# Performance work log

Hardware: AMD Instinct MI355X
Metric: run time of the kernel (lower is better)

Reference implementation:

```python
import jax, jax.numpy as jnp
import numpy as np

D_QUERY = 512
D_AUDIO = 512
D_OUT = 512
B, HW, S = 16, 4096, 1024


def setup_inputs() -> dict:
    key = jax.random.key(0)
    ks = jax.random.split(key, 8)
    sc_q = 1.0 / np.sqrt(D_QUERY)
    sc_a = 1.0 / np.sqrt(D_AUDIO)
    return {
        "x": jax.random.normal(ks[0], (B, HW, D_QUERY), dtype=jnp.float32),
        "audio_embed": jax.random.normal(ks[1], (B, S, D_AUDIO), dtype=jnp.float32),
        "Wq": jax.random.uniform(ks[2], (D_QUERY, D_OUT), jnp.float32, -sc_q, sc_q),
        "bq": jax.random.uniform(ks[3], (D_OUT,), jnp.float32, -sc_q, sc_q),
        "Wk": jax.random.uniform(ks[4], (D_AUDIO, D_OUT), jnp.float32, -sc_a, sc_a),
        "bk": jax.random.uniform(ks[5], (D_OUT,), jnp.float32, -sc_a, sc_a),
        "Wv": jax.random.uniform(ks[6], (D_AUDIO, D_OUT), jnp.float32, -sc_a, sc_a),
        "bv": jax.random.uniform(ks[7], (D_OUT,), jnp.float32, -sc_a, sc_a),
    }


def reference(x, audio_embed, Wq, bq, Wk, bk, Wv, bv):
    # Linear projections (nn.Linear: y = x @ W^T + b; we store W already transposed)
    Q = x @ Wq + bq                      # [B, HW, D_OUT]
    K = audio_embed @ Wk + bk            # [B, S, D_OUT]
    V = audio_embed @ Wv + bv            # [B, S, D_OUT]
    scale = 1.0 / (K.shape[-1] ** 0.5)   # divide by sqrt(d_out), per source
    scores = jnp.einsum("bnd,bsd->bns", Q, K) * scale  # [B, HW, S]
    attn = jax.nn.softmax(scores, axis=-1)
    return jnp.einsum("bns,bsd->bnd", attn, V)         # [B, HW, D_OUT]
```

## Files before the change

kernel.cpp:

```cpp
#include <hip/hip_runtime.h>
#include <hip/hip_bf16.h>

typedef __attribute__((ext_vector_type(8))) short bf16x8;
typedef __attribute__((ext_vector_type(4))) float f32x4;
typedef __attribute__((ext_vector_type(4))) unsigned short ushort4v;

#define AS1 __attribute__((address_space(1)))
#define AS3 __attribute__((address_space(3)))

__device__ __forceinline__ float bf_bits_to_f(short s) {
  unsigned int u = ((unsigned int)(unsigned short)s) << 16;
  union { unsigned int u; float f; } c; c.u = u; return c.f;
}
__device__ __forceinline__ unsigned short f_to_bf_bits(float f) {
  union { float f; unsigned int u; } c; c.f = f;
  unsigned int r = c.u + 0x7FFFu + ((c.u >> 16) & 1u);
  return (unsigned short)(r >> 16);
}

__device__ __forceinline__ int fsw(int row) { return ((row >> 1) & 3) << 4; }

__global__ __launch_bounds__(256) void cvt_bf16_kernel(const float* __restrict__ in,
                                                       unsigned short* __restrict__ out,
                                                       long n) {
  const long nchunks = n >> 2;
  const long stride = (long)gridDim.x * 256;
  for (long c = (long)blockIdx.x * 256 + threadIdx.x; c < nchunks; c += stride) {
    f32x4 v = *(const f32x4*)(in + c * 4);
    ushort4v o;
    o[0] = f_to_bf_bits(v[0]); o[1] = f_to_bf_bits(v[1]);
    o[2] = f_to_bf_bits(v[2]); o[3] = f_to_bf_bits(v[3]);
    *(ushort4v*)(out + c * 4) = o;
  }
}

__global__ __launch_bounds__(256) void transpose1_kernel(
    const float* __restrict__ W, unsigned short* __restrict__ T) {
  __shared__ float t[32][33];
  const int tx = threadIdx.x & 31, ty = threadIdx.x >> 5;
  const int n0 = blockIdx.x * 32, k0 = blockIdx.y * 32;
#pragma unroll
  for (int j = 0; j < 4; ++j)
    t[ty + 8 * j][tx] = W[(long)(k0 + ty + 8 * j) * 512 + n0 + tx];
  __syncthreads();
#pragma unroll
  for (int j = 0; j < 4; ++j)
    T[(long)(n0 + ty + 8 * j) * 512 + k0 + tx] = f_to_bf_bits(t[tx][ty + 8 * j]);
}

__global__ __launch_bounds__(256) void wvec_kernel(const float* __restrict__ Wk,
                                                   const float* __restrict__ bq,
                                                   float* __restrict__ w, const float s) {
  const int q = blockIdx.x * 4 + (threadIdx.x >> 6);
  const int lane = threadIdx.x & 63;
  const float* row = Wk + (long)q * 512 + lane * 8;
  const f32x4 a0 = *(const f32x4*)row;
  const f32x4 a1 = *(const f32x4*)(row + 4);
  const f32x4 b0 = *(const f32x4*)(bq + lane * 8);
  const f32x4 b1 = *(const f32x4*)(bq + lane * 8 + 4);
  float d = a0[0]*b0[0] + a0[1]*b0[1] + a0[2]*b0[2] + a0[3]*b0[3]
          + a1[0]*b1[0] + a1[1]*b1[1] + a1[2]*b1[2] + a1[3]*b1[3];
  for (int off = 1; off < 64; off <<= 1) d += __shfl_xor(d, off);
  if (lane == 0) w[q] = d * s;
}

__global__ __launch_bounds__(256) void cvec_kernel(const float* __restrict__ audio,
                                                   const float* __restrict__ w,
                                                   float* __restrict__ cv) {
  const long row = (long)blockIdx.x * 4 + (threadIdx.x >> 6);
  const int lane = threadIdx.x & 63;
  const f32x4 a0 = *(const f32x4*)(audio + row * 512 + lane * 8);
  const f32x4 a1 = *(const f32x4*)(audio + row * 512 + lane * 8 + 4);
  const f32x4 w0 = *(const f32x4*)(w + lane * 8);
  const f32x4 w1 = *(const f32x4*)(w + lane * 8 + 4);
  float d = a0[0]*w0[0] + a0[1]*w0[1] + a0[2]*w0[2] + a0[3]*w0[3]
          + a1[0]*w1[0] + a1[1]*w1[1] + a1[2]*w1[2] + a1[3]*w1[3];
  for (int off = 1; off < 64; off <<= 1) d += __shfl_xor(d, off);
  if (lane == 0) cv[row] = d;
}

template <bool BIAS, bool TRANSOUT, bool AFP32>
__global__ __launch_bounds__(256) void gemm_kernel(
    const void* __restrict__ Aptr,
    const unsigned short* __restrict__ BT,
    const float* __restrict__ bias,
    unsigned short* __restrict__ Cout,
    const int K, const float scale,
    const long strideA, const long strideBT, const long strideC, const int ldc,
    const int nx, const int ny) {
  __shared__ unsigned short lds[8192];
  const int nwg = gridDim.x;
  const int chunk = nwg >> 3;
  const int bid = blockIdx.x;
  const int swz = (bid & 7) * chunk + (bid >> 3);
  const int bx = swz % nx;
  const int t1 = swz / nx;
  const int by = t1 % ny;
  const int bz = t1 / ny;

  const int tid = threadIdx.x;
  const int lane = tid & 63;
  const int wv = tid >> 6;
  const int wr = wv >> 1, wc = wv & 1;
  const unsigned short* Ab = (const unsigned short*)Aptr + (long)bz * strideA + (long)by * 128 * K;
  const float* Af = (const float*)Aptr + (long)bz * strideA + (long)by * 128 * K;
  const unsigned short* Bb = BT + (long)bz * strideBT + (long)bx * 128 * K;

  f32x4 acc[4][4];
#pragma unroll
  for (int m = 0; m < 4; ++m)
#pragma unroll
    for (int n = 0; n < 4; ++n) acc[m][n] = (f32x4){0.f, 0.f, 0.f, 0.f};

  const int r15 = lane & 15, g = lane >> 4;
  const int kiters = K >> 5;
  const int asw = fsw(r15);

  int arow[2], acs[2];
#pragma unroll
  for (int i = 0; i < 2; ++i) {
    const int c = i * 4 + wv;
    const int boff = c * 1024 + lane * 16;
    arow[i] = boff >> 6;
    acs[i] = (boff & 63) ^ fsw(arow[i]);
  }
  f32x4 pa[2][2];
  if (AFP32) {
#pragma unroll
    for (int i = 0; i < 2; ++i) {
      const float* s = Af + (long)arow[i] * K + (acs[i] >> 1);
      pa[i][0] = *(const f32x4*)s;
      pa[i][1] = *(const f32x4*)(s + 4);
    }
  }

  for (int kt = 0; kt < kiters; ++kt) {
#pragma unroll
    for (int i = 0; i < 2; ++i) {
      const int c = i * 4 + wv;
      const char* srcB = (const char*)Bb + (long)arow[i] * (K * 2) + kt * 64 + acs[i];
      __builtin_amdgcn_global_load_lds(
          (const AS1 void*)srcB, (AS3 void*)(lds + 4096 + c * 512), 16, 0, 0);
      if (!AFP32) {
        const char* srcA = (const char*)Ab + (long)arow[i] * (K * 2) + kt * 64 + acs[i];
        __builtin_amdgcn_global_load_lds(
            (const AS1 void*)srcA, (AS3 void*)(lds + c * 512), 16, 0, 0);
      }
    }
    if (AFP32) {
#pragma unroll
      for (int i = 0; i < 2; ++i) {
        const int c = i * 4 + wv;
        bf16x8 w;
#pragma unroll
        for (int e = 0; e < 4; ++e) {
          w[e] = (short)f_to_bf_bits(pa[i][0][e]);
          w[4 + e] = (short)f_to_bf_bits(pa[i][1][e]);
        }
        *(bf16x8*)&lds[c * 512 + lane * 8] = w;
      }
      if (kt < kiters - 1) {
#pragma unroll
        for (int i = 0; i < 2; ++i) {
          const float* s = Af + (long)arow[i] * K + (kt + 1) * 32 + (acs[i] >> 1);
          pa[i][0] = *(const f32x4*)s;
          pa[i][1] = *(const f32x4*)(s + 4);
        }
      }
    }
    __syncthreads();

    bf16x8 af[4], bf[4];
#pragma unroll
    for (int m = 0; m < 4; ++m)
      af[m] = *(const bf16x8*)((const char*)lds + (wr * 64 + m * 16 + r15) * 64 + (g * 16 ^ asw));
#pragma unroll
    for (int n = 0; n < 4; ++n)
      bf[n] = *(const bf16x8*)((const char*)lds + 8192 +
                               (wc * 64 + n * 16 + r15) * 64 + (g * 16 ^ asw));
#pragma unroll
    for (int m = 0; m < 4; ++m)
#pragma unroll
      for (int n = 0; n < 4; ++n)
        acc[m][n] = __builtin_amdgcn_mfma_f32_16x16x32_bf16(af[m], bf[n], acc[m][n], 0, 0, 0);
    __syncthreads();
  }

  const long crow0 = (long)by * 128 + wr * 64;
  const long ccol0 = (long)bx * 128 + wc * 64;
#pragma unroll
  for (int n = 0; n < 4; ++n) {
    const long col = ccol0 + n * 16 + r15;
    const float bv = BIAS ? bias[col] : 0.f;
#pragma unroll
    for (int m = 0; m < 4; ++m) {
      const f32x4 v = acc[m][n];
#pragma unroll
      for (int j = 0; j < 4; ++j) {
        const long row = crow0 + m * 16 + g * 4 + j;
        const float val = (v[j] + bv) * scale;
        const long idx = TRANSOUT ? (col * (long)ldc + row) : (row * (long)ldc + col);
        (Cout + (long)bz * strideC)[idx] = f_to_bf_bits(val);
      }
    }
  }
}

__global__ __launch_bounds__(256) void projdual_kernel(
    const float* __restrict__ audio,
    const unsigned short* __restrict__ wvt,
    const unsigned short* __restrict__ G,
    const float* __restrict__ bv,
    unsigned short* __restrict__ Vt,
    unsigned short* __restrict__ KMb) {
  __shared__ unsigned short lds[8192];
  const int nwg = gridDim.x;
  const int chunk = nwg >> 3;
  const int bid = blockIdx.x;
  const int swz = (bid & 7) * chunk + (bid >> 3);
  const int bx = swz & 7;
  const int t1 = swz >> 3;
  const int by = t1 & 7;
  const int bz = t1 >> 3;

  const int tid = threadIdx.x;
  const int lane = tid & 63;
  const int wv = tid >> 6;
  const int wr = wv >> 1, wc = wv & 1;
  const float* Af = audio + (long)bz * 1024 * 512 + (long)by * 128 * 512;
  const unsigned short* Bb = (bx < 4) ? (wvt + (long)bx * 128 * 512)
                                      : (G + (long)(bx - 4) * 128 * 512);

  f32x4 acc[4][4];
#pragma unroll
  for (int m = 0; m < 4; ++m)
#pragma unroll
    for (int n = 0; n < 4; ++n) acc[m][n] = (f32x4){0.f, 0.f, 0.f, 0.f};

  const int r15 = lane & 15, g = lane >> 4;
  const int asw = fsw(r15);

  int arow[2], acs[2];
#pragma unroll
  for (int i = 0; i < 2; ++i) {
    const int c = i * 4 + wv;
    const int boff = c * 1024 + lane * 16;
    arow[i] = boff >> 6;
    acs[i] = (boff & 63) ^ fsw(arow[i]);
  }
  f32x4 pa[2][2];
#pragma unroll
  for (int i = 0; i < 2; ++i) {
    const float* s = Af + (long)arow[i] * 512 + (acs[i] >> 1);
    pa[i][0] = *(const f32x4*)s;
    pa[i][1] = *(const f32x4*)(s + 4);
  }

  for (int kt = 0; kt < 16; ++kt) {
#pragma unroll
    for (int i = 0; i < 2; ++i) {
      const int c = i * 4 + wv;
      const char* srcB = (const char*)Bb + (long)arow[i] * 1024 + kt * 64 + acs[i];
      __builtin_amdgcn_global_load_lds(
          (const AS1 void*)srcB, (AS3 void*)(lds + 4096 + c * 512), 16, 0, 0);
    }
#pragma unroll
    for (int i = 0; i < 2; ++i) {
      const int c = i * 4 + wv;
      bf16x8 w;
#pragma unroll
      for (int e = 0; e < 4; ++e) {
        w[e] = (short)f_to_bf_bits(pa[i][0][e]);
        w[4 + e] = (short)f_to_bf_bits(pa[i][1][e]);
      }
      *(bf16x8*)&lds[c * 512 + lane * 8] = w;
    }
    if (kt < 15) {
#pragma unroll
      for (int i = 0; i < 2; ++i) {
        const float* s = Af + (long)arow[i] * 512 + (kt + 1) * 32 + (acs[i] >> 1);
        pa[i][0] = *(const f32x4*)s;
        pa[i][1] = *(const f32x4*)(s + 4);
      }
    }
    __syncthreads();

    bf16x8 af[4], bf[4];
#pragma unroll
    for (int m = 0; m < 4; ++m)
      af[m] = *(const bf16x8*)((const char*)lds + (wr * 64 + m * 16 + r15) * 64 + (g * 16 ^ asw));
#pragma unroll
    for (int n = 0; n < 4; ++n)
      bf[n] = *(const bf16x8*)((const char*)lds + 8192 +
                               (wc * 64 + n * 16 + r15) * 64 + (g * 16 ^ asw));
#pragma unroll
    for (int m = 0; m < 4; ++m)
#pragma unroll
      for (int n = 0; n < 4; ++n)
        acc[m][n] = __builtin_amdgcn_mfma_f32_16x16x32_bf16(af[m], bf[n], acc[m][n], 0, 0, 0);
    __syncthreads();
  }

  const long crow0 = (long)by * 128 + wr * 64;
  const long ccol0 = (long)bx * 128 + wc * 64;
#pragma unroll
  for (int n = 0; n < 4; ++n) {
    const long col = ccol0 + n * 16 + r15;
    const float bvv = (bx < 4) ? bv[col] : 0.f;
#pragma unroll
    for (int m = 0; m < 4; ++m) {
      const f32x4 v = acc[m][n];
#pragma unroll
      for (int j = 0; j < 4; ++j) {
        const long row = crow0 + m * 16 + g * 4 + j;
        const float val = v[j] + bvv;
        if (bx < 4)
          Vt[(long)bz * 512 * 1024 + col * 1024 + row] = f_to_bf_bits(val);
        else
          KMb[(long)bz * 1024 * 512 + row * 512 + (col - 512)] = f_to_bf_bits(val);
      }
    }
  }
}

template <bool EXPSTATS, bool DIVSTATS>
__global__ __launch_bounds__(512, 2) void gemm256_kernel(
    const unsigned short* __restrict__ A,
    const unsigned short* __restrict__ BT,
    void* __restrict__ Cout,
    const int K,
    const long strideA, const long strideBT, const long strideC, const int ldc,
    const int nx, const int ny, float* __restrict__ stats,
    const float* __restrict__ cbias) {
  __shared__ __align__(16) char halfb[4][32768];
  __shared__ float ssum[256][4];
  __shared__ float invl[256];

  const int nwg = gridDim.x;
  const int chunk = nwg >> 3;
  const int bid = blockIdx.x;
  const int swz = (bid & 7) * chunk + (bid >> 3);
  const int bx = swz % nx;
  const int t1 = swz / nx;
  const int by = t1 % ny;
  const int bz = t1 / ny;

  const int tid = threadIdx.x;
  const int lane = tid & 63;
  const int w = tid >> 6;
  const int wm = w >> 2, wn = w & 3;
  const int r15 = lane & 15, g = lane >> 4;
  const int asw = fsw(r15);

  const char* Abyt = (const char*)(A + (long)bz * strideA + (long)by * 256 * K);
  const char* Bbyt = (const char*)(BT + (long)bz * strideBT + (long)bx * 256 * K);
  const long rsb = (long)K * 2;

  if (DIVSTATS) {
    if (tid < 256) {
      const f32x4 s = *(const f32x4*)&stats[((long)bz * 4096 + (long)by * 256 + tid) * 4];
      invl[tid] = 1.f / (s[0] + s[1] + s[2] + s[3]);
    }
  }
  __builtin_amdgcn_sched_barrier(0);

  const int srow0 = tid >> 2;
  const int scol = ((tid & 3) << 4) ^ fsw(srow0);
  const long aoff0 = (long)srow0 * rsb + scol;
  const long aoff1 = (long)(srow0 + 128) * rsb + scol;
  const int dbase = tid * 16;

  auto stage = [&](int s) {
    char* h = halfb[s & 3];
    const long kb = (long)s * 64;
    __builtin_amdgcn_global_load_lds((const AS1 void*)(Abyt + aoff0 + kb),
                                     (AS3 void*)(h + dbase), 16, 0, 0);
    __builtin_amdgcn_global_load_lds((const AS1 void*)(Abyt + aoff1 + kb),
                                     (AS3 void*)(h + 8192 + dbase), 16, 0, 0);
    __builtin_amdgcn_global_load_lds((const AS1 void*)(Bbyt + aoff0 + kb),
                                     (AS3 void*)(h + 16384 + dbase), 16, 0, 0);
    __builtin_amdgcn_global_load_lds((const AS1 void*)(Bbyt + aoff1 + kb),
                                     (AS3 void*)(h + 24576 + dbase), 16, 0, 0);
  };

  f32x4 acc[8][4];
#pragma unroll
  for (int m = 0; m < 8; ++m)
#pragma unroll
    for (int n = 0; n < 4; ++n) acc[m][n] = (f32x4){0.f, 0.f, 0.f, 0.f};

  const int kslices = K >> 5;

  stage(0);
  stage(1);
  stage(2);
  asm volatile("s_waitcnt vmcnt(8)" ::: "memory");
  __builtin_amdgcn_s_barrier();
  __builtin_amdgcn_sched_barrier(0);

  for (int s = 0; s < kslices; ++s) {
    const char* hA = halfb[s & 3];
    const char* hB = halfb[s & 3] + 16384;
    bf16x8 fa[8], fb[4];
#pragma unroll
    for (int m = 0; m < 8; ++m)
      fa[m] = *(const bf16x8*)(hA + (wm * 128 + m * 16 + r15) * 64 + ((g * 16) ^ asw));
#pragma unroll
    for (int n = 0; n < 4; ++n)
      fb[n] = *(const bf16x8*)(hB + (wn * 64 + n * 16 + r15) * 64 + ((g * 16) ^ asw));
    __builtin_amdgcn_sched_barrier(0);
    if (s < kslices - 2) asm volatile("s_waitcnt vmcnt(4)" ::: "memory");
    else                 asm volatile("s_waitcnt vmcnt(0)" ::: "memory");
    __builtin_amdgcn_s_barrier();
    asm volatile("s_waitcnt lgkmcnt(0)" ::: "memory");
    __builtin_amdgcn_sched_barrier(0);
    if (s + 3 < kslices) stage(s + 3);
    __builtin_amdgcn_s_setprio(1);
#pragma unroll
    for (int m = 0; m < 8; ++m)
#pragma unroll
      for (int n = 0; n < 4; ++n)
        acc[m][n] = __builtin_amdgcn_mfma_f32_16x16x32_bf16(fa[m], fb[n], acc[m][n], 0, 0, 0);
    __builtin_amdgcn_s_setprio(0);
    __builtin_amdgcn_sched_barrier(0);
  }

  if (EXPSTATS) {
    float cb[4];
#pragma unroll
    for (int n = 0; n < 4; ++n)
      cb[n] = cbias[(long)bz * 1024 + (long)bx * 256 + wn * 64 + n * 16 + r15];
#pragma unroll
    for (int m = 0; m < 8; ++m)
#pragma unroll
      for (int n = 0; n < 4; ++n)
#pragma unroll
        for (int j = 0; j < 4; ++j) acc[m][n][j] = __expf(acc[m][n][j] + cb[n]);
#pragma unroll
    for (int m = 0; m < 8; ++m)
#pragma unroll
      for (int j = 0; j < 4; ++j) {
        float s = acc[m][0][j] + acc[m][1][j] + acc[m][2][j] + acc[m][3][j];
        s += __shfl_xor(s, 1);
        s += __shfl_xor(s, 2);
        s += __shfl_xor(s, 4);
        s += __shfl_xor(s, 8);
        if (r15 == 0) ssum[wm * 128 + m * 16 + g * 4 + j][wn] = s;
      }
    __syncthreads();
    if (tid < 256) {
      const float t = ssum[tid][0] + ssum[tid][1] + ssum[tid][2] + ssum[tid][3];
      stats[((long)bz * 4096 + (long)by * 256 + tid) * 4 + bx] = t;
    }
  }

  const long crow0 = (long)by * 256 + wm * 128;
  const long ccol0 = (long)bx * 256 + wn * 64;
#pragma unroll
  for (int m = 0; m < 8; ++m)
#pragma unroll
    for (int j = 0; j < 4; ++j) {
      const int rl = wm * 128 + m * 16 + g * 4 + j;
      const long row = crow0 + m * 16 + g * 4 + j;
#pragma unroll
      for (int n = 0; n < 4; ++n) {
        const long col = ccol0 + n * 16 + r15;
        if (EXPSTATS) {
          ((unsigned short*)Cout + (long)bz * strideC)[row * (long)ldc + col] =
              f_to_bf_bits(acc[m][n][j]);
        } else {
          const float sc = DIVSTATS ? invl[rl] : 1.f;
          ((float*)Cout + (long)bz * strideC)[row * (long)ldc + col] = acc[m][n][j] * sc;
        }
      }
    }
}

extern "C" void kernel_launch(void* const* d_in, const int* in_sizes, int n_in,
                              void* d_out, int out_size, void* d_ws, size_t ws_size,
                              hipStream_t stream) {
  (void)in_sizes; (void)n_in; (void)out_size; (void)ws_size;
  const float* x     = (const float*)d_in[0];
  const float* audio = (const float*)d_in[1];
  const float* Wq    = (const float*)d_in[2];
  const float* bq    = (const float*)d_in[3];
  const float* Wk    = (const float*)d_in[4];
  const float* bk    = (const float*)d_in[5];  (void)bk;
  const float* Wv    = (const float*)d_in[6];
  const float* bv    = (const float*)d_in[7];
  float* out = (float*)d_out;

  const float s = 0.044194173824159216f;

  char* ws = (char*)d_ws;
  size_t off = 0;
  auto carve = [&](size_t bytes) { char* p = ws + off; off += (bytes + 255) & ~(size_t)255; return p; };
  unsigned short* xb  = (unsigned short*)carve((size_t)65536 * 512 * 2);
  unsigned short* wkb = (unsigned short*)carve((size_t)512 * 512 * 2);
  unsigned short* wvt = (unsigned short*)carve((size_t)512 * 512 * 2);
  unsigned short* G   = (unsigned short*)carve((size_t)512 * 512 * 2);
  unsigned short* KMb = (unsigned short*)carve((size_t)16384 * 512 * 2);
  unsigned short* Vt  = (unsigned short*)carve((size_t)16384 * 512 * 2);
  unsigned short* Pb  = (unsigned short*)carve((size_t)65536 * 1024 * 2);
  float*          ls  = (float*)carve((size_t)65536 * 4 * 4);
  float*          wv_ = (float*)carve((size_t)512 * 4);
  float*          cv  = (float*)carve((size_t)16384 * 4);

  cvt_bf16_kernel<<<2048, 256, 0, stream>>>(x, xb, (long)65536 * 512);
  cvt_bf16_kernel<<<256, 256, 0, stream>>>(Wk, wkb, (long)512 * 512);
  transpose1_kernel<<<dim3(16, 16), 256, 0, stream>>>(Wv, wvt);
  gemm_kernel<false, false, true><<<16, 256, 0, stream>>>(
      Wq, wkb, nullptr, G, 512, s, 0, 0, 0, 512, 4, 4);
  wvec_kernel<<<128, 256, 0, stream>>>(Wk, bq, wv_, s);
  cvec_kernel<<<4096, 256, 0, stream>>>(audio, wv_, cv);
  projdual_kernel<<<8 * 8 * 16, 256, 0, stream>>>(audio, wvt, G, bv, Vt, KMb);
  gemm256_kernel<true, false><<<4 * 16 * 16, 512, 0, stream>>>(
      xb, KMb, Pb, 512,
      (long)4096 * 512, (long)1024 * 512, (long)4096 * 1024, 1024, 4, 16, ls, cv);
  gemm256_kernel<false, true><<<2 * 16 * 16, 512, 0, stream>>>(
      Pb, Vt, out, 1024,
      (long)4096 * 1024, (long)512 * 1024, (long)4096 * 512, 512, 2, 16, ls, nullptr);
}
```

Measured before the change: 342.1 us.

## Merge small prep kernels and co-schedule x conversion with projection GEMM

The Wk conversion, Wv transpose and wvec dot product are folded into one prep kernel selected by block index. The x-to-bf16 conversion and the cvec reduction become extra block ranges of the projection GEMM launch, so the bandwidth-bound conversion can run alongside the compute-bound projection tiles. This cuts the launch count from eight to four and removes the gaps between them. In exchange the swizzle is hard-coded to 1024 GEMM blocks, and the mixed block types may compete for CUs and bandwidth.

```diff
diff --git a/kernel.cpp b/kernel.cpp
--- a/kernel.cpp
+++ b/kernel.cpp
@@ -20,63 +20,43 @@
 
 __device__ __forceinline__ int fsw(int row) { return ((row >> 1) & 3) << 4; }
 
-__global__ __launch_bounds__(256) void cvt_bf16_kernel(const float* __restrict__ in,
-                                                       unsigned short* __restrict__ out,
-                                                       long n) {
-  const long nchunks = n >> 2;
-  const long stride = (long)gridDim.x * 256;
-  for (long c = (long)blockIdx.x * 256 + threadIdx.x; c < nchunks; c += stride) {
-    f32x4 v = *(const f32x4*)(in + c * 4);
+__global__ __launch_bounds__(256) void prep_kernel(
+    const float* __restrict__ Wk, const float* __restrict__ Wv,
+    const float* __restrict__ bq,
+    unsigned short* __restrict__ wkb, unsigned short* __restrict__ wvt,
+    float* __restrict__ w, const float s) {
+  const int bi = blockIdx.x;
+  if (bi < 256) {
+    __shared__ float t[32][33];
+    const int tx = threadIdx.x & 31, ty = threadIdx.x >> 5;
+    const int n0 = (bi & 15) * 32, k0 = (bi >> 4) * 32;
+#pragma unroll
+    for (int j = 0; j < 4; ++j)
+      t[ty + 8 * j][tx] = Wv[(long)(k0 + ty + 8 * j) * 512 + n0 + tx];
+    __syncthreads();
+#pragma unroll
+    for (int j = 0; j < 4; ++j)
+      wvt[(long)(n0 + ty + 8 * j) * 512 + k0 + tx] = f_to_bf_bits(t[tx][ty + 8 * j]);
+  } else if (bi < 512) {
+    const long c = (long)(bi - 256) * 256 + threadIdx.x;
+    const f32x4 v = *(const f32x4*)(Wk + c * 4);
     ushort4v o;
     o[0] = f_to_bf_bits(v[0]); o[1] = f_to_bf_bits(v[1]);
     o[2] = f_to_bf_bits(v[2]); o[3] = f_to_bf_bits(v[3]);
-    *(ushort4v*)(out + c * 4) = o;
-  }
-}
-
-__global__ __launch_bounds__(256) void transpose1_kernel(
-    const float* __restrict__ W, unsigned short* __restrict__ T) {
-  __shared__ float t[32][33];
-  const int tx = threadIdx.x & 31, ty = threadIdx.x >> 5;
-  const int n0 = blockIdx.x * 32, k0 = blockIdx.y * 32;
-#pragma unroll
-  for (int j = 0; j < 4; ++j)
-    t[ty + 8 * j][tx] = W[(long)(k0 + ty + 8 * j) * 512 + n0 + tx];
-  __syncthreads();
-#pragma unroll
-  for (int j = 0; j < 4; ++j)
-    T[(long)(n0 + ty + 8 * j) * 512 + k0 + tx] = f_to_bf_bits(t[tx][ty + 8 * j]);
-}
-
-__global__ __launch_bounds__(256) void wvec_kernel(const float* __restrict__ Wk,
-                                                   const float* __restrict__ bq,
-                                                   float* __restrict__ w, const float s) {
-  const int q = blockIdx.x * 4 + (threadIdx.x >> 6);
-  const int lane = threadIdx.x & 63;
-  const float* row = Wk + (long)q * 512 + lane * 8;
-  const f32x4 a0 = *(const f32x4*)row;
-  const f32x4 a1 = *(const f32x4*)(row + 4);
-  const f32x4 b0 = *(const f32x4*)(bq + lane * 8);
-  const f32x4 b1 = *(const f32x4*)(bq + lane * 8 + 4);
-  float d = a0[0]*b0[0] + a0[1]*b0[1] + a0[2]*b0[2] + a0[3]*b0[3]
-          + a1[0]*b1[0] + a1[1]*b1[1] + a1[2]*b1[2] + a1[3]*b1[3];
-  for (int off = 1; off < 64; off <<= 1) d += __shfl_xor(d, off);
-  if (lane == 0) w[q] = d * s;
-}
-
-__global__ __launch_bounds__(256) void cvec_kernel(const float* __restrict__ audio,
-                                                   const float* __restrict__ w,
-                                                   float* __restrict__ cv) {
-  const long row = (long)blockIdx.x * 4 + (threadIdx.x >> 6);
-  const int lane = threadIdx.x & 63;
-  const f32x4 a0 = *(const f32x4*)(audio + row * 512 + lane * 8);
-  const f32x4 a1 = *(const f32x4*)(audio + row * 512 + lane * 8 + 4);
-  const f32x4 w0 = *(const f32x4*)(w + lane * 8);
-  const f32x4 w1 = *(const f32x4*)(w + lane * 8 + 4);
-  float d = a0[0]*w0[0] + a0[1]*w0[1] + a0[2]*w0[2] + a0[3]*w0[3]
-          + a1[0]*w1[0] + a1[1]*w1[1] + a1[2]*w1[2] + a1[3]*w1[3];
-  for (int off = 1; off < 64; off <<= 1) d += __shfl_xor(d, off);
-  if (lane == 0) cv[row] = d;
+    *(ushort4v*)(wkb + c * 4) = o;
+  } else {
+    const int q = (bi - 512) * 4 + (threadIdx.x >> 6);
+    const int lane = threadIdx.x & 63;
+    const float* row = Wk + (long)q * 512 + lane * 8;
+    const f32x4 a0 = *(const f32x4*)row;
+    const f32x4 a1 = *(const f32x4*)(row + 4);
+    const f32x4 b0 = *(const f32x4*)(bq + lane * 8);
+    const f32x4 b1 = *(const f32x4*)(bq + lane * 8 + 4);
+    float d = a0[0]*b0[0] + a0[1]*b0[1] + a0[2]*b0[2] + a0[3]*b0[3]
+            + a1[0]*b1[0] + a1[1]*b1[1] + a1[2]*b1[2] + a1[3]*b1[3];
+    for (int off = 1; off < 64; off <<= 1) d += __shfl_xor(d, off);
+    if (lane == 0) w[q] = d * s;
+  }
 }
 
 template <bool BIAS, bool TRANSOUT, bool AFP32>
@@ -206,24 +186,53 @@
   }
 }
 
-__global__ __launch_bounds__(256) void projdual_kernel(
+__global__ __launch_bounds__(256) void projfuse_kernel(
     const float* __restrict__ audio,
     const unsigned short* __restrict__ wvt,
     const unsigned short* __restrict__ G,
     const float* __restrict__ bv,
+    const float* __restrict__ x,
+    const float* __restrict__ w,
     unsigned short* __restrict__ Vt,
-    unsigned short* __restrict__ KMb) {
+    unsigned short* __restrict__ KMb,
+    unsigned short* __restrict__ xb,
+    float* __restrict__ cv) {
   __shared__ unsigned short lds[8192];
-  const int nwg = gridDim.x;
-  const int chunk = nwg >> 3;
   const int bid = blockIdx.x;
-  const int swz = (bid & 7) * chunk + (bid >> 3);
+  const int tid = threadIdx.x;
+
+  if (bid >= 2048) {
+    const int lane = tid & 63;
+    for (long row = (long)(bid - 2048) * 4 + (tid >> 6); row < 16384; row += 1024) {
+      const f32x4 a0 = *(const f32x4*)(audio + row * 512 + lane * 8);
+      const f32x4 a1 = *(const f32x4*)(audio + row * 512 + lane * 8 + 4);
+      const f32x4 w0 = *(const f32x4*)(w + lane * 8);
+      const f32x4 w1 = *(const f32x4*)(w + lane * 8 + 4);
+      float d = a0[0]*w0[0] + a0[1]*w0[1] + a0[2]*w0[2] + a0[3]*w0[3]
+              + a1[0]*w1[0] + a1[1]*w1[1] + a1[2]*w1[2] + a1[3]*w1[3];
+      for (int off = 1; off < 64; off <<= 1) d += __shfl_xor(d, off);
+      if (lane == 0) cv[row] = d;
+    }
+    return;
+  }
+  if (bid >= 1024) {
+    const long nchunks = (long)65536 * 512 / 4;
+    for (long c = (long)(bid - 1024) * 256 + tid; c < nchunks; c += 262144) {
+      const f32x4 v = *(const f32x4*)(x + c * 4);
+      ushort4v o;
+      o[0] = f_to_bf_bits(v[0]); o[1] = f_to_bf_bits(v[1]);
+      o[2] = f_to_bf_bits(v[2]); o[3] = f_to_bf_bits(v[3]);
+      *(ushort4v*)(xb + c * 4) = o;
+    }
+    return;
+  }
+
+  const int swz = (bid & 7) * 128 + (bid >> 3);
   const int bx = swz & 7;
   const int t1 = swz >> 3;
   const int by = t1 & 7;
   const int bz = t1 >> 3;
 
-  const int tid = threadIdx.x;
   const int lane = tid & 63;
   const int wv = tid >> 6;
   const int wr = wv >> 1, wc = wv & 1;
@@ -251,9 +260,9 @@
   f32x4 pa[2][2];
 #pragma unroll
   for (int i = 0; i < 2; ++i) {
-    const float* s = Af + (long)arow[i] * 512 + (acs[i] >> 1);
-    pa[i][0] = *(const f32x4*)s;
-    pa[i][1] = *(const f32x4*)(s + 4);
+    const float* sp = Af + (long)arow[i] * 512 + (acs[i] >> 1);
+    pa[i][0] = *(const f32x4*)sp;
+    pa[i][1] = *(const f32x4*)(sp + 4);
   }
 
   for (int kt = 0; kt < 16; ++kt) {
@@ -267,20 +276,20 @@
 #pragma unroll
     for (int i = 0; i < 2; ++i) {
       const int c = i * 4 + wv;
-      bf16x8 w;
+      bf16x8 wq;
 #pragma unroll
       for (int e = 0; e < 4; ++e) {
-        w[e] = (short)f_to_bf_bits(pa[i][0][e]);
-        w[4 + e] = (short)f_to_bf_bits(pa[i][1][e]);
-      }
-      *(bf16x8*)&lds[c * 512 + lane * 8] = w;
+        wq[e] = (short)f_to_bf_bits(pa[i][0][e]);
+        wq[4 + e] = (short)f_to_bf_bits(pa[i][1][e]);
+      }
+      *(bf16x8*)&lds[c * 512 + lane * 8] = wq;
     }
     if (kt < 15) {
 #pragma unroll
       for (int i = 0; i < 2; ++i) {
-        const float* s = Af + (long)arow[i] * 512 + (kt + 1) * 32 + (acs[i] >> 1);
-        pa[i][0] = *(const f32x4*)s;
-        pa[i][1] = *(const f32x4*)(s + 4);
+        const float* sp = Af + (long)arow[i] * 512 + (kt + 1) * 32 + (acs[i] >> 1);
+        pa[i][0] = *(const f32x4*)sp;
+        pa[i][1] = *(const f32x4*)(sp + 4);
       }
     }
     __syncthreads();
@@ -506,14 +515,10 @@
   float*          wv_ = (float*)carve((size_t)512 * 4);
   float*          cv  = (float*)carve((size_t)16384 * 4);
 
-  cvt_bf16_kernel<<<2048, 256, 0, stream>>>(x, xb, (long)65536 * 512);
-  cvt_bf16_kernel<<<256, 256, 0, stream>>>(Wk, wkb, (long)512 * 512);
-  transpose1_kernel<<<dim3(16, 16), 256, 0, stream>>>(Wv, wvt);
+  prep_kernel<<<640, 256, 0, stream>>>(Wk, Wv, bq, wkb, wvt, wv_, s);
   gemm_kernel<false, false, true><<<16, 256, 0, stream>>>(
       Wq, wkb, nullptr, G, 512, s, 0, 0, 0, 512, 4, 4);
-  wvec_kernel<<<128, 256, 0, stream>>>(Wk, bq, wv_, s);
-  cvec_kernel<<<4096, 256, 0, stream>>>(audio, wv_, cv);
-  projdual_kernel<<<8 * 8 * 16, 256, 0, stream>>>(audio, wvt, G, bv, Vt, KMb);
+  projfuse_kernel<<<2304, 256, 0, stream>>>(audio, wvt, G, bv, x, wv_, Vt, KMb, xb, cv);
   gemm256_kernel<true, false><<<4 * 16 * 16, 512, 0, stream>>>(
       xb, KMb, Pb, 512,
       (long)4096 * 512, (long)1024 * 512, (long)4096 * 1024, 1024, 4, 16, ls, cv);
```

After: 336.8 us. Within noise of the previous version (-1.6%).
